# Optimization experiments

Measured on AMD Instinct MI355X. Metric: run time of the kernel, lower is better.

## Reference

```python
import jax, jax.numpy as jnp
import numpy as np

N_NODES = 50000
N_EDGES = 600000
EMBED_DIM = 128


def setup_inputs() -> dict:
    key = jax.random.key(0)
    k1, k2 = jax.random.split(key)
    x = jax.random.normal(k1, (N_NODES, EMBED_DIM), dtype=jnp.float32)
    edge_index = jax.random.randint(k2, (2, N_EDGES), 0, N_NODES, dtype=jnp.int64)
    bias = jnp.zeros((EMBED_DIM,), dtype=jnp.float32)
    return {"x": x, "edge_index": edge_index, "bias": bias}


def reference(x, edge_index, bias):
    # init_embedding is Identity (disable_init_embedding=True)
    init_embeds = x
    n = x.shape[0]
    # add_self_loops
    loops = jnp.arange(n, dtype=edge_index.dtype)
    row = jnp.concatenate([edge_index[0], loops])  # source nodes
    col = jnp.concatenate([edge_index[1], loops])  # destination nodes
    # degree of destination nodes
    deg = jax.ops.segment_sum(jnp.ones_like(col, dtype=x.dtype), col, num_segments=n)
    deg_inv_sqrt = jnp.where(deg > 0, jax.lax.rsqrt(jnp.maximum(deg, 1e-20)), 0.0)
    # symmetric GCN normalization per edge
    norm = deg_inv_sqrt[row] * deg_inv_sqrt[col]  # [E+N]
    # message: gather source features, scale, scatter-add into destinations
    msg = norm[:, None] * x[row]  # [E+N, D]
    out = jax.ops.segment_sum(msg, col, num_segments=n) + bias
    return (out, init_embeds)
```

## Files before the change

### kernel.cpp

```cpp
#include <hip/hip_runtime.h>

#define D 128
#define B 256
#define WMAX 64
#define SPILL_MAX 8192
#define UPL 4

typedef float vfloat4 __attribute__((ext_vector_type(4)));


__device__ __forceinline__ unsigned short f2bf(float f) {
    unsigned u = __float_as_uint(f);
    u = u + 0x7FFFu + ((u >> 16) & 1u);
    return (unsigned short)(u >> 16);
}

__device__ __forceinline__ vfloat4 bf2f4(uint2 v) {
    vfloat4 r;
    r.x = __uint_as_float(v.x << 16);
    r.y = __uint_as_float(v.x & 0xffff0000u);
    r.z = __uint_as_float(v.y << 16);
    r.w = __uint_as_float(v.y & 0xffff0000u);
    return r;
}

__global__ void k_prep(const float* __restrict__ x, float* __restrict__ out2,
                       uint2* __restrict__ xb, int* __restrict__ cursor,
                       int* __restrict__ spillCnt, int n) {
    int gid = blockIdx.x * blockDim.x + threadIdx.x;
    if (gid == 0) *spillCnt = 0;
    if (gid < n) cursor[gid] = 0;
    if (gid >= n * 32) return;
    vfloat4 xv = reinterpret_cast<const vfloat4*>(x)[gid];
    __builtin_nontemporal_store(xv, reinterpret_cast<vfloat4*>(out2) + gid);
    uint2 b;
    b.x = (unsigned)f2bf(xv.x) | ((unsigned)f2bf(xv.y) << 16);
    b.y = (unsigned)f2bf(xv.z) | ((unsigned)f2bf(xv.w) << 16);
    xb[gid] = b;
}

__global__ void k_place_ell(const int* __restrict__ row, const int* __restrict__ col,
                            int* __restrict__ cursor, int* __restrict__ ssrc,
                            int2* __restrict__ spill, int* __restrict__ spillCnt, int e) {
    int t = blockIdx.x * blockDim.x + threadIdx.x;
    int T = gridDim.x * blockDim.x;

    int r[UPL], c[UPL], p[UPL];
#pragma unroll
    for (int u = 0; u < UPL; ++u) {
        int i = t + u * T;
        bool v = (i < e);
        r[u] = v ? row[i] : -1;
        c[u] = v ? col[i] : 0;
    }
#pragma unroll
    for (int u = 0; u < UPL; ++u)
        p[u] = (r[u] >= 0) ? atomicAdd(&cursor[c[u]], 1) : 0;
#pragma unroll
    for (int u = 0; u < UPL; ++u) {
        if (r[u] < 0) continue;
        if (p[u] < WMAX) {
            ssrc[c[u] * WMAX + p[u]] = r[u];
        } else {
            int s = atomicAdd(spillCnt, 1);
            if (s < SPILL_MAX) spill[s] = make_int2(r[u], c[u]);
        }
    }
}

__global__ void k_agg_ell(const uint2* __restrict__ xb, const float* __restrict__ bias,
                          const int* __restrict__ cursor, const int* __restrict__ ssrc,
                          const int2* __restrict__ spill, const int* __restrict__ spillCnt,
                          float* __restrict__ out, int n) {
    int gid = blockIdx.x * blockDim.x + threadIdx.x;
    if (gid >= n * 32) return;
    int node = gid >> 5;
    int q    = gid & 31;

    int cnt = cursor[node];
    int m   = min(cnt, WMAX);
    const int* sp = ssrc + node * WMAX;

    vfloat4 a0 = {0.f, 0.f, 0.f, 0.f};
    vfloat4 a1 = a0, a2 = a0, a3 = a0;

    int j = 0;
    for (; j + 4 <= m; j += 4) {
        int r0 = sp[j + 0], r1 = sp[j + 1], r2 = sp[j + 2], r3 = sp[j + 3];
        uint2 v0 = xb[(size_t)r0 * 32 + q];
        uint2 v1 = xb[(size_t)r1 * 32 + q];
        uint2 v2 = xb[(size_t)r2 * 32 + q];
        uint2 v3 = xb[(size_t)r3 * 32 + q];
        float w0 = rsqrtf((float)cursor[r0] + 1.0f);
        float w1 = rsqrtf((float)cursor[r1] + 1.0f);
        float w2 = rsqrtf((float)cursor[r2] + 1.0f);
        float w3 = rsqrtf((float)cursor[r3] + 1.0f);
        a0 += w0 * bf2f4(v0);
        a1 += w1 * bf2f4(v1);
        a2 += w2 * bf2f4(v2);
        a3 += w3 * bf2f4(v3);
    }
    for (; j < m; ++j) {
        int r = sp[j];
        uint2 v = xb[(size_t)r * 32 + q];
        float w = rsqrtf((float)cursor[r] + 1.0f);
        a0 += w * bf2f4(v);
    }

    if (cnt > WMAX) {
        int sc = min(*spillCnt, SPILL_MAX);
        for (int s = 0; s < sc; ++s) {
            int2 pr = spill[s];
            if (pr.y == node) {
                float w = rsqrtf((float)cursor[pr.x] + 1.0f);
                a0 += w * bf2f4(xb[(size_t)pr.x * 32 + q]);
            }
        }
    }

    float dc = rsqrtf((float)cnt + 1.0f);
    vfloat4 xc = bf2f4(xb[(size_t)node * 32 + q]);
    vfloat4 bv = reinterpret_cast<const vfloat4*>(bias)[q];
    vfloat4 ov = bv + dc * (a0 + a1 + a2 + a3 + dc * xc);

    __builtin_nontemporal_store(ov, reinterpret_cast<vfloat4*>(out) + (size_t)node * 32 + q);
}


__global__ void k_zero(int* __restrict__ degInt, int n) {
    int i = blockIdx.x * blockDim.x + threadIdx.x;
    if (i < n) degInt[i] = 0;
}

__global__ void k_count(const int* __restrict__ col, int* __restrict__ degInt, int e) {
    int i = blockIdx.x * blockDim.x + threadIdx.x;
    if (i < e) atomicAdd(&degInt[col[i]], 1);
}

__global__ void k_scan1(const int* __restrict__ degInt, int* __restrict__ off,
                        int* __restrict__ bsum, int n) {
    __shared__ int sm[B];
    int i = blockIdx.x * B + threadIdx.x;
    int v = (i < n) ? degInt[i] : 0;
    sm[threadIdx.x] = v;
    __syncthreads();
    for (int s = 1; s < B; s <<= 1) {
        int t = (threadIdx.x >= (unsigned)s) ? sm[threadIdx.x - s] : 0;
        __syncthreads();
        sm[threadIdx.x] += t;
        __syncthreads();
    }
    if (i < n) off[i] = sm[threadIdx.x] - v;
    if (threadIdx.x == B - 1) bsum[blockIdx.x] = sm[B - 1];
}

__global__ void k_scan2(int* __restrict__ bsum, int nb) {
    __shared__ int sm[B];
    int v = (threadIdx.x < (unsigned)nb) ? bsum[threadIdx.x] : 0;
    sm[threadIdx.x] = v;
    __syncthreads();
    for (int s = 1; s < B; s <<= 1) {
        int t = (threadIdx.x >= (unsigned)s) ? sm[threadIdx.x - s] : 0;
        __syncthreads();
        sm[threadIdx.x] += t;
        __syncthreads();
    }
    if (threadIdx.x < (unsigned)nb) bsum[threadIdx.x] = sm[threadIdx.x] - v;
}

__global__ void k_scan3(int* __restrict__ off, const int* __restrict__ bsum,
                        const int* __restrict__ degInt, float* __restrict__ dis,
                        int* __restrict__ cursor, int n, int e) {
    int i = blockIdx.x * B + threadIdx.x;
    if (i < n) {
        int o = off[i] + bsum[blockIdx.x];
        off[i] = o;
        cursor[i] = o;
        dis[i] = rsqrtf((float)degInt[i] + 1.0f);
    }
    if (i == 0) off[n] = e;
}

__global__ void k_place_pairs(const int* __restrict__ row, const int* __restrict__ col,
                              const float* __restrict__ dis, int* __restrict__ cursor,
                              int2* __restrict__ pairs, int e) {
    int i = blockIdx.x * blockDim.x + threadIdx.x;
    if (i >= e) return;
    int r = row[i];
    int c = col[i];
    float w = dis[r];
    int pos = atomicAdd(&cursor[c], 1);
    pairs[pos] = make_int2(r, __float_as_int(w));
}

__global__ void k_aggregate_pairs(const float* __restrict__ x, const float* __restrict__ bias,
                                  const float* __restrict__ dis, const int* __restrict__ off,
                                  const int2* __restrict__ pairs, float* __restrict__ out,
                                  float* __restrict__ out2, int n) {
    int gid = blockIdx.x * blockDim.x + threadIdx.x;
    if (gid >= n * 32) return;
    int node = gid >> 5;
    int q    = gid & 31;
    const vfloat4* x4 = reinterpret_cast<const vfloat4*>(x);
    int j   = off[node];
    int end = off[node + 1];
    vfloat4 a0 = {0.f, 0.f, 0.f, 0.f};
    vfloat4 a1 = a0, a2 = a0, a3 = a0;
    for (; j + 4 <= end; j += 4) {
        int2 p0 = pairs[j + 0];
        int2 p1 = pairs[j + 1];
        int2 p2 = pairs[j + 2];
        int2 p3 = pairs[j + 3];
        vfloat4 v0 = x4[(size_t)p0.x * 32 + q];
        vfloat4 v1 = x4[(size_t)p1.x * 32 + q];
        vfloat4 v2 = x4[(size_t)p2.x * 32 + q];
        vfloat4 v3 = x4[(size_t)p3.x * 32 + q];
        a0 += __int_as_float(p0.y) * v0;
        a1 += __int_as_float(p1.y) * v1;
        a2 += __int_as_float(p2.y) * v2;
        a3 += __int_as_float(p3.y) * v3;
    }
    for (; j < end; ++j) {
        int2 p = pairs[j];
        a0 += __int_as_float(p.y) * x4[(size_t)p.x * 32 + q];
    }
    float dc = dis[node];
    vfloat4 xc = x4[(size_t)node * 32 + q];
    vfloat4 bv = reinterpret_cast<const vfloat4*>(bias)[q];
    vfloat4 ov = bv + dc * (a0 + a1 + a2 + a3 + dc * xc);
    __builtin_nontemporal_store(ov, reinterpret_cast<vfloat4*>(out)  + (size_t)node * 32 + q);
    __builtin_nontemporal_store(xc, reinterpret_cast<vfloat4*>(out2) + (size_t)node * 32 + q);
}


extern "C" void kernel_launch(void* const* d_in, const int* in_sizes, int n_in,
                              void* d_out, int out_size, void* d_ws, size_t ws_size,
                              hipStream_t stream) {
    const float* x    = (const float*)d_in[0];
    const int*   idx  = (const int*)d_in[1];
    const float* bias = (const float*)d_in[2];

    const int n = in_sizes[0] / D;
    const int e = in_sizes[1] / 2;

    const int* row = idx;
    const int* col = idx + e;

    float* out  = (float*)d_out;
    float* out2 = (float*)d_out + (size_t)n * D;

    const int nbN = (n + B - 1) / B;
    const int nbE = (e + B - 1) / B;
    const int aggB = (n * 32 + B - 1) / B;

    char* p0 = (char*)d_ws;
    int*  cursor  = (int*)p0;                        p0 += (size_t)n * 4;
    int*  spillCnt= (int*)p0;                        p0 += 16;
    int2* spill   = (int2*)p0;                       p0 += (size_t)SPILL_MAX * 8;
    p0 = (char*)(((uintptr_t)p0 + 15) & ~(uintptr_t)15);
    uint2* xb     = (uint2*)p0;                      p0 += (size_t)n * 32 * 8;
    int*  ssrc    = (int*)p0;                        p0 += (size_t)n * WMAX * 4;
    size_t need_ell = (size_t)(p0 - (char*)d_ws);

    if (ws_size >= need_ell) {
        const int plB = (e + B * UPL - 1) / (B * UPL);
        k_prep     <<<aggB, B, 0, stream>>>(x, out2, xb, cursor, spillCnt, n);
        k_place_ell<<<plB,  B, 0, stream>>>(row, col, cursor, ssrc, spill, spillCnt, e);
        k_agg_ell  <<<aggB, B, 0, stream>>>(xb, bias, cursor, ssrc, spill, spillCnt, out, n);
        return;
    }

    char* p = (char*)d_ws;
    int*   degInt = (int*)p;            p += (size_t)n * 4;
    int*   cur2   = (int*)p;            p += (size_t)n * 4;
    int*   off    = (int*)p;            p += (size_t)(n + 1) * 4;
    int*   bsum   = (int*)p;            p += 256 * 4;
    float* dis    = (float*)p;          p += (size_t)n * 4;
    p = (char*)(((uintptr_t)p + 15) & ~(uintptr_t)15);
    int2*  pairs  = (int2*)p;

    k_zero <<<nbN, B, 0, stream>>>(degInt, n);
    k_count<<<nbE, B, 0, stream>>>(col, degInt, e);
    k_scan1<<<nbN, B, 0, stream>>>(degInt, off, bsum, n);
    k_scan2<<<1,   B, 0, stream>>>(bsum, nbN);
    k_scan3<<<nbN, B, 0, stream>>>(off, bsum, degInt, dis, cur2, n, e);
    k_place_pairs<<<nbE, B, 0, stream>>>(row, col, dis, cur2, pairs, e);
    k_aggregate_pairs<<<aggB, B, 0, stream>>>(x, bias, dis, off, pairs, out, out2, n);
}
```

Measured before the change: 81.91 us.

## Partition edge placement and aggregation by destination range across XCD-interleaved blocks

```diff
diff --git a/kernel.cpp b/kernel.cpp
--- a/kernel.cpp
+++ b/kernel.cpp
@@ -4,7 +4,7 @@
 #define B 256
 #define WMAX 64
 #define SPILL_MAX 8192
-#define UPL 4
+#define NPART 8
 
 typedef float vfloat4 __attribute__((ext_vector_type(4)));
 
@@ -41,29 +41,25 @@
 
 __global__ void k_place_ell(const int* __restrict__ row, const int* __restrict__ col,
                             int* __restrict__ cursor, int* __restrict__ ssrc,
-                            int2* __restrict__ spill, int* __restrict__ spillCnt, int e) {
-    int t = blockIdx.x * blockDim.x + threadIdx.x;
-    int T = gridDim.x * blockDim.x;
-
-    int r[UPL], c[UPL], p[UPL];
-#pragma unroll
-    for (int u = 0; u < UPL; ++u) {
-        int i = t + u * T;
-        bool v = (i < e);
-        r[u] = v ? row[i] : -1;
-        c[u] = v ? col[i] : 0;
-    }
-#pragma unroll
-    for (int u = 0; u < UPL; ++u)
-        p[u] = (r[u] >= 0) ? atomicAdd(&cursor[c[u]], 1) : 0;
-#pragma unroll
-    for (int u = 0; u < UPL; ++u) {
-        if (r[u] < 0) continue;
-        if (p[u] < WMAX) {
-            ssrc[c[u] * WMAX + p[u]] = r[u];
+                            int2* __restrict__ spill, int* __restrict__ spillCnt,
+                            int e, int n) {
+    int p  = blockIdx.x & (NPART - 1);
+    int bg = blockIdx.x >> 3;
+    int tg = bg * blockDim.x + threadIdx.x;
+    int T  = (gridDim.x >> 3) * blockDim.x;
+    int lo = (int)((long long)n * p / NPART);
+    int hi = (int)((long long)n * (p + 1) / NPART);
+
+    for (int i = tg; i < e; i += T) {
+        int c = col[i];
+        if (c < lo || c >= hi) continue;
+        int r = row[i];
+        int pos = atomicAdd(&cursor[c], 1);
+        if (pos < WMAX) {
+            ssrc[c * WMAX + pos] = r;
         } else {
             int s = atomicAdd(spillCnt, 1);
-            if (s < SPILL_MAX) spill[s] = make_int2(r[u], c[u]);
+            if (s < SPILL_MAX) spill[s] = make_int2(r, c);
         }
     }
 }
@@ -72,10 +68,11 @@
                           const int* __restrict__ cursor, const int* __restrict__ ssrc,
                           const int2* __restrict__ spill, const int* __restrict__ spillCnt,
                           float* __restrict__ out, int n) {
-    int gid = blockIdx.x * blockDim.x + threadIdx.x;
-    if (gid >= n * 32) return;
-    int node = gid >> 5;
-    int q    = gid & 31;
+    int bpg = (gridDim.x + NPART - 1) >> 3;
+    int node_block = (blockIdx.x & (NPART - 1)) * bpg + (blockIdx.x >> 3);
+    int node = node_block * 8 + (threadIdx.x >> 5);
+    if (node >= n) return;
+    int q = threadIdx.x & 31;
 
     int cnt = cursor[node];
     int m   = min(cnt, WMAX);
@@ -263,10 +260,12 @@
     size_t need_ell = (size_t)(p0 - (char*)d_ws);
 
     if (ws_size >= need_ell) {
-        const int plB = (e + B * UPL - 1) / (B * UPL);
+        const int plB = 2048;
+        const int bpg  = (n + 8 * NPART - 1) / (8 * NPART);
+        const int agB  = bpg * NPART;
         k_prep     <<<aggB, B, 0, stream>>>(x, out2, xb, cursor, spillCnt, n);
-        k_place_ell<<<plB,  B, 0, stream>>>(row, col, cursor, ssrc, spill, spillCnt, e);
-        k_agg_ell  <<<aggB, B, 0, stream>>>(xb, bias, cursor, ssrc, spill, spillCnt, out, n);
+        k_place_ell<<<plB,  B, 0, stream>>>(row, col, cursor, ssrc, spill, spillCnt, e, n);
+        k_agg_ell  <<<agB,  B, 0, stream>>>(xb, bias, cursor, ssrc, spill, spillCnt, out, n);
         return;
     }
 
```

New measurement: 77.10 us. 1.06x faster.
